# Performance work log

Hardware: AMD Instinct MI355X
Metric: run time of the kernel (lower is better)

Reference implementation:

```python
import jax, jax.numpy as jnp
import numpy as np


def setup_inputs() -> dict:
    ks = iter(jax.random.split(jax.random.key(0), 32))
    B, L, Dm = 16, 256, 512          # batch, seq_len (== len_size), d_model
    N, K, R = 16, 4, 32              # d_state, d_conv, dt_rank = ceil(512/16)
    DI = 2 * Dm                      # d_inner = expand * d_model
    nrm = lambda shape, s=0.02: jax.random.normal(next(ks), shape, jnp.float32) * s
    return {
        "x": jax.random.normal(next(ks), (B, L, Dm), jnp.float32),
        "x_key": jax.random.normal(next(ks), (B, Dm), jnp.float32),
        "in_proj_w": nrm((Dm, 2 * DI)),
        "conv_w": nrm((DI, K), 0.3),                 # depthwise conv kernel
        "conv_b": jnp.zeros((DI,), jnp.float32),
        "x_proj_w": nrm((DI, R + 2 * N)),
        "x_proj_b_w": nrm((DI, R + 2 * N)),
        "x_proj_s_w": nrm((DI, R + 2 * DI)),
        "dt_w": nrm((R, DI)), "dt_bias": jnp.zeros((DI,), jnp.float32),
        "dt_b_w": nrm((R, DI)), "dt_b_bias": jnp.zeros((DI,), jnp.float32),
        "dt_s_w": nrm((R, DI)), "dt_s_bias": jnp.zeros((DI,), jnp.float32),
        "key1_w": nrm((Dm, DI)),
        "key2_w": nrm((N,), 0.1),                    # Linear(1, d_state), no bias
        "keys_w": nrm((Dm, L)),                      # Linear(d_model, len_size)
        "A_log": jnp.log(jnp.arange(1, N + 1, dtype=jnp.float32))[None, :],
        "A_b_log": jnp.log(jnp.arange(1, N + 1, dtype=jnp.float32))[None, :],
        "A_s_log": jnp.log(jnp.arange(1, DI + 1, dtype=jnp.float32))[None, :],
        "D": jnp.ones((DI,), jnp.float32),
        "D_b": jnp.ones((DI,), jnp.float32),
        "D_s": jnp.ones((DI,), jnp.float32),
        "out_proj_w": nrm((DI, Dm)),
    }


def reference(x, x_key, in_proj_w, conv_w, conv_b, x_proj_w, x_proj_b_w, x_proj_s_w,
              dt_w, dt_bias, dt_b_w, dt_b_bias, dt_s_w, dt_s_bias,
              key1_w, key2_w, keys_w, A_log, A_b_log, A_s_log,
              D, D_b, D_s, out_proj_w):
    B, L, _ = x.shape
    R = dt_w.shape[0]
    N = A_log.shape[1]
    DI, K = conv_w.shape

    xz = x @ in_proj_w                                # (B,L,2*DI)
    xc, res = jnp.split(xz, 2, axis=-1)

    # causal depthwise conv (torch pads both sides by K-1 then slices [:L])
    xp = jnp.pad(xc, ((0, 0), (K - 1, 0), (0, 0)))
    u = conv_b + sum(xp[:, k:k + L, :] * conv_w[:, k] for k in range(K))
    u = jax.nn.silu(u)                                # (B,L,DI)

    def proj(W, n):
        p = u @ W
        return jnp.split(p, [R, R + n], axis=-1)

    dr, Bm, Cm = proj(x_proj_w, N)
    drb, Bb, Cb = proj(x_proj_b_w, N)
    drs, Bs, Cs = proj(x_proj_s_w, DI)
    delta = jax.nn.softplus(dr @ dt_w + dt_bias)      # (B,L,DI)
    delta_b = jax.nn.softplus(drb @ dt_b_w + dt_b_bias)
    delta_s = jax.nn.softplus(drs @ dt_s_w + dt_s_bias)

    A = -jnp.exp(A_log[0])                            # (N,)
    Ab = -jnp.exp(A_b_log[0])
    As = -jnp.exp(A_s_log[0])                         # (DI,)

    # initial state: key_proj_2(key_proj_1(x_key)[:, :, None]) -> (B,DI,N)
    s0 = (x_key @ key1_w)[:, :, None] * key2_w

    def temporal(dlt, Aa, Bi, Ci, Dd, reverse):
        dA = jnp.exp(dlt[..., None] * Aa)                           # (B,L,DI,N)
        dBu = dlt[..., None] * Bi[:, :, None, :] * u[..., None]    # (B,L,DI,N)

        def step(s, inp):
            dA_t, dBu_t, C_t = inp
            s = dA_t * s + dBu_t
            return s, jnp.einsum('bdn,bn->bd', s, C_t)

        xs = (jnp.moveaxis(dA, 1, 0), jnp.moveaxis(dBu, 1, 0), jnp.moveaxis(Ci, 1, 0))
        _, ys = jax.lax.scan(step, s0, xs, reverse=reverse)
        return jnp.moveaxis(ys, 0, 1) + u * Dd

    y_f = temporal(delta, A, Bm, Cm, D, False)
    y_b = temporal(delta_b, Ab, Bb, Cb, D_b, True)

    # spatial scan: recurrence over the channel axis, state over sequence positions.
    # torch einsum 'b l d, d n -> b l n' with A_s (1,DI) broadcasts then sums d:
    dA_s = jnp.exp(jnp.sum(delta_s, -1, keepdims=True) * As)        # (B,L,DI)
    dBu_s = jnp.sum(delta_s * u, -1, keepdims=True) * Bs            # (B,L,DI)

    def sstep(s, inp):
        a, bb, c = inp
        s = a * s + bb
        return s, s * c

    _, ys_s = jax.lax.scan(
        sstep, x_key @ keys_w,
        (jnp.moveaxis(dA_s, 2, 0), jnp.moveaxis(dBu_s, 2, 0), jnp.moveaxis(Cs, 2, 0)))
    y_s = jnp.moveaxis(ys_s, 0, 2) + u * D_s                        # (B,L,DI)

    y = y_f + y_b + y_s + res
    return y @ out_proj_w
```

## Files before the change

### kernel.cpp

```cpp
#include <hip/hip_runtime.h>
#include <cstddef>
#include <cstdint>

#define B_   16
#define L_   256
#define DM_  512
#define DI_  1024
#define N_   16
#define R_   32
#define K_   4
#define ROWS (B_ * L_)
#define PP_  256

typedef __attribute__((ext_vector_type(8))) short bf16x8;
typedef __attribute__((ext_vector_type(4))) float f32x4;

__device__ inline unsigned short f2bf(float x) {
    unsigned u = __float_as_uint(x);
    unsigned r = u + 0x7FFFu + ((u >> 16) & 1u);
    return (unsigned short)(r >> 16);
}
__device__ inline float bf2f(unsigned short h) {
    return __uint_as_float(((unsigned)h) << 16);
}

__device__ inline float rowsum16(float x) {
    x += __uint_as_float(__builtin_amdgcn_update_dpp(0, __float_as_uint(x), 0x118, 0xf, 0xf, true));
    x += __uint_as_float(__builtin_amdgcn_update_dpp(0, __float_as_uint(x), 0x114, 0xf, 0xf, true));
    x += __uint_as_float(__builtin_amdgcn_update_dpp(0, __float_as_uint(x), 0x112, 0xf, 0xf, true));
    x += __uint_as_float(__builtin_amdgcn_update_dpp(0, __float_as_uint(x), 0x111, 0xf, 0xf, true));
    return x;
}

#define BM 128
#define BN 128
#define BK 16

__global__ __launch_bounds__(256)
void gemm_f32(const float* __restrict__ A, const float* __restrict__ W,
              float* __restrict__ C, const float* __restrict__ bias,
              int M, int N, int K, int lda, int ldw, int ldc, int mode)
{
    __shared__ float As[BK][BM + 4];
    __shared__ float Ws[BK][BN + 4];
    const int tid = threadIdx.x;
    const int bn = blockIdx.x * BN;
    const int bm = blockIdx.y * BM;

    const int arow = tid >> 2;
    const int ak   = (tid & 3) * 4;
    const int wrow = tid >> 4;
    const int wc   = (tid & 15) * 8;
    const int tx = tid & 15, ty = tid >> 4;

    float acc[8][8];
    #pragma unroll
    for (int i = 0; i < 8; ++i)
        #pragma unroll
        for (int j = 0; j < 8; ++j) acc[i][j] = 0.f;

    for (int kt = 0; kt < K; kt += BK) {
        #pragma unroll
        for (int h = 0; h < 2; ++h) {
            int r = arow + h * 64;
            int grow = bm + r;
            float4 v = make_float4(0.f, 0.f, 0.f, 0.f);
            if (grow < M)
                v = *reinterpret_cast<const float4*>(A + (size_t)grow * lda + kt + ak);
            As[ak + 0][r] = v.x; As[ak + 1][r] = v.y;
            As[ak + 2][r] = v.z; As[ak + 3][r] = v.w;
        }
        #pragma unroll
        for (int h = 0; h < 2; ++h) {
            int col = wc + h * 4;
            int gcol = bn + col;
            float4 v;
            if (gcol + 3 < N) {
                v = *reinterpret_cast<const float4*>(W + (size_t)(kt + wrow) * ldw + gcol);
            } else {
                float t0 = (gcol + 0 < N) ? W[(size_t)(kt + wrow) * ldw + gcol + 0] : 0.f;
                float t1 = (gcol + 1 < N) ? W[(size_t)(kt + wrow) * ldw + gcol + 1] : 0.f;
                float t2 = (gcol + 2 < N) ? W[(size_t)(kt + wrow) * ldw + gcol + 2] : 0.f;
                float t3 = (gcol + 3 < N) ? W[(size_t)(kt + wrow) * ldw + gcol + 3] : 0.f;
                v = make_float4(t0, t1, t2, t3);
            }
            *reinterpret_cast<float4*>(&Ws[wrow][col]) = v;
        }
        __syncthreads();
        #pragma unroll
        for (int k = 0; k < BK; ++k) {
            float av[8], wv[8];
            #pragma unroll
            for (int i = 0; i < 8; ++i) av[i] = As[k][ty * 8 + i];
            #pragma unroll
            for (int j = 0; j < 8; ++j) wv[j] = Ws[k][tx * 8 + j];
            #pragma unroll
            for (int i = 0; i < 8; ++i)
                #pragma unroll
                for (int j = 0; j < 8; ++j)
                    acc[i][j] = fmaf(av[i], wv[j], acc[i][j]);
        }
        __syncthreads();
    }

    #pragma unroll
    for (int i = 0; i < 8; ++i) {
        int r = bm + ty * 8 + i;
        if (r >= M) break;
        #pragma unroll
        for (int j = 0; j < 8; ++j) {
            int cc = bn + tx * 8 + j;
            if (cc < N) {
                float v = acc[i][j];
                if (mode == 1) {
                    v += bias[cc];
                    v = fmaxf(v, 0.f) + log1pf(__expf(-fabsf(v)));
                }
                C[(size_t)r * ldc + cc] = v;
            }
        }
    }
}

#define SBM 128
#define SBN 128
#define SBK 32
#define SLDK 40

__global__ __launch_bounds__(256)
void gemm_split_mfma(const unsigned short* __restrict__ Ahi, const unsigned short* __restrict__ Alo,
                     const unsigned short* __restrict__ Bthi, const unsigned short* __restrict__ Btlo,
                     float* __restrict__ C, int M, int N, int K)
{
    __shared__ unsigned short sAh[SBM][SLDK], sAl[SBM][SLDK];
    __shared__ unsigned short sBh[SBN][SLDK], sBl[SBN][SLDK];
    const int tid = threadIdx.x;
    const int bm = blockIdx.y * SBM;
    const int bn = blockIdx.x * SBN;
    const int w = tid >> 6, lane = tid & 63;
    const int wr = w >> 1, wc = w & 1;
    const int lr = lane & 15, kg = lane >> 4;

    f32x4 acc[4][4];
    #pragma unroll
    for (int i = 0; i < 4; ++i)
        #pragma unroll
        for (int j = 0; j < 4; ++j) acc[i][j] = (f32x4){0.f, 0.f, 0.f, 0.f};

    const int srow0 = tid >> 2;
    const int sks   = (tid & 3) * 8;

    for (int kt = 0; kt < K; kt += SBK) {
        #pragma unroll
        for (int h = 0; h < 2; ++h) {
            int r = srow0 + h * 64;
            size_t ga = (size_t)(bm + r) * K + kt + sks;
            size_t gb = (size_t)(bn + r) * K + kt + sks;
            uint4 vah = *reinterpret_cast<const uint4*>(Ahi + ga);
            uint4 val = *reinterpret_cast<const uint4*>(Alo + ga);
            uint4 vbh = *reinterpret_cast<const uint4*>(Bthi + gb);
            uint4 vbl = *reinterpret_cast<const uint4*>(Btlo + gb);
            *reinterpret_cast<uint4*>(&sAh[r][sks]) = vah;
            *reinterpret_cast<uint4*>(&sAl[r][sks]) = val;
            *reinterpret_cast<uint4*>(&sBh[r][sks]) = vbh;
            *reinterpret_cast<uint4*>(&sBl[r][sks]) = vbl;
        }
        __syncthreads();

        bf16x8 ah[4], al[4], bh[4], bl[4];
        #pragma unroll
        for (int i = 0; i < 4; ++i) {
            ah[i] = *reinterpret_cast<const bf16x8*>(&sAh[wr * 64 + i * 16 + lr][kg * 8]);
            al[i] = *reinterpret_cast<const bf16x8*>(&sAl[wr * 64 + i * 16 + lr][kg * 8]);
            bh[i] = *reinterpret_cast<const bf16x8*>(&sBh[wc * 64 + i * 16 + lr][kg * 8]);
            bl[i] = *reinterpret_cast<const bf16x8*>(&sBl[wc * 64 + i * 16 + lr][kg * 8]);
        }
        #pragma unroll
        for (int i = 0; i < 4; ++i)
            #pragma unroll
            for (int j = 0; j < 4; ++j) {
                acc[i][j] = __builtin_amdgcn_mfma_f32_16x16x32_bf16(ah[i], bh[j], acc[i][j], 0, 0, 0);
                acc[i][j] = __builtin_amdgcn_mfma_f32_16x16x32_bf16(ah[i], bl[j], acc[i][j], 0, 0, 0);
                acc[i][j] = __builtin_amdgcn_mfma_f32_16x16x32_bf16(al[i], bh[j], acc[i][j], 0, 0, 0);
            }
        __syncthreads();
    }

    #pragma unroll
    for (int i = 0; i < 4; ++i)
        #pragma unroll
        for (int j = 0; j < 4; ++j) {
            int col = bn + wc * 64 + j * 16 + lr;
            int rb  = bm + wr * 64 + i * 16 + kg * 4;
            #pragma unroll
            for (int r = 0; r < 4; ++r)
                C[(size_t)(rb + r) * N + col] = acc[i][j][r];
        }
}

__global__ __launch_bounds__(256)
void split_f32(const float* __restrict__ in, unsigned short* __restrict__ hi,
               unsigned short* __restrict__ lo, int n4)
{
    int i = blockIdx.x * 256 + threadIdx.x;
    if (i >= n4) return;
    float4 v = reinterpret_cast<const float4*>(in)[i];
    ushort4 h, l;
    h.x = f2bf(v.x); l.x = f2bf(v.x - bf2f(h.x));
    h.y = f2bf(v.y); l.y = f2bf(v.y - bf2f(h.y));
    h.z = f2bf(v.z); l.z = f2bf(v.z - bf2f(h.z));
    h.w = f2bf(v.w); l.w = f2bf(v.w - bf2f(h.w));
    reinterpret_cast<ushort4*>(hi)[i] = h;
    reinterpret_cast<ushort4*>(lo)[i] = l;
}

__global__ __launch_bounds__(256)
void split_transpose(const float* __restrict__ W, int ldw, int rows, int cols,
                     unsigned short* __restrict__ Thi, unsigned short* __restrict__ Tlo)
{
    __shared__ float t[32][33];
    int k0 = blockIdx.y * 32, n0 = blockIdx.x * 32;
    int tx = threadIdx.x, ty = threadIdx.y;
    #pragma unroll
    for (int i = 0; i < 4; ++i)
        t[ty + i * 8][tx] = W[(size_t)(k0 + ty + i * 8) * ldw + n0 + tx];
    __syncthreads();
    #pragma unroll
    for (int i = 0; i < 4; ++i) {
        int n = ty + i * 8;
        float v = t[tx][n];
        unsigned short h = f2bf(v);
        Thi[(size_t)(n0 + n) * rows + k0 + tx] = h;
        Tlo[(size_t)(n0 + n) * rows + k0 + tx] = f2bf(v - bf2f(h));
    }
}

__global__ __launch_bounds__(256)
void proj_wT(const float* __restrict__ xw, const float* __restrict__ xbw,
             const float* __restrict__ xsw,
             unsigned short* __restrict__ Th, unsigned short* __restrict__ Tl)
{
    int idx = blockIdx.x * 256 + threadIdx.x;
    int k = idx & (DI_ - 1);
    int j = idx >> 10;
    float v = 0.f;
    if (j < 64)       v = xw[(size_t)k * 64 + j];
    else if (j < 128) v = xbw[(size_t)k * 64 + (j - 64)];
    else if (j < 160) v = xsw[(size_t)k * (R_ + 2 * DI_) + (j - 128)];
    unsigned short h = f2bf(v);
    Th[(size_t)j * DI_ + k] = h;
    Tl[(size_t)j * DI_ + k] = f2bf(v - bf2f(h));
}

__global__ __launch_bounds__(256)
void init_state(const float* __restrict__ x_key, const float* __restrict__ key1_w,
                const float* __restrict__ keys_w, float* __restrict__ xk1,
                float* __restrict__ s0sp)
{
    int b = blockIdx.y;
    int col = blockIdx.x * 256 + threadIdx.x;
    __shared__ float xk[DM_];
    for (int i = threadIdx.x; i < DM_; i += 256) xk[i] = x_key[b * DM_ + i];
    __syncthreads();
    float acc = 0.f;
    if (col < DI_) {
        for (int k = 0; k < DM_; ++k)
            acc = fmaf(xk[k], key1_w[(size_t)k * DI_ + col], acc);
        xk1[b * DI_ + col] = acc;
    } else {
        int c = col - DI_;
        for (int k = 0; k < DM_; ++k)
            acc = fmaf(xk[k], keys_w[(size_t)k * L_ + c], acc);
        s0sp[b * L_ + c] = acc;
    }
}

__global__ __launch_bounds__(256)
void conv_silu(const float* __restrict__ xz, const float* __restrict__ conv_w,
               const float* __restrict__ conv_b, float* __restrict__ u)
{
    int idx = blockIdx.x * 256 + threadIdx.x;
    if (idx >= ROWS * DI_) return;
    int d  = idx & (DI_ - 1);
    int rl = idx >> 10;
    int l  = rl & (L_ - 1);
    float acc = conv_b[d];
    #pragma unroll
    for (int k = 0; k < K_; ++k) {
        int ll = l + k - (K_ - 1);
        if (ll >= 0)
            acc = fmaf(xz[(size_t)(rl + k - (K_ - 1)) * (2 * DI_) + d], conv_w[d * K_ + k], acc);
    }
    u[idx] = acc / (1.f + __expf(-acc));
}

__global__ __launch_bounds__(256)
void init_yacc(const float* __restrict__ xz, const float* __restrict__ u,
               const float* __restrict__ D, const float* __restrict__ Db,
               const float* __restrict__ Ds, float* __restrict__ yacc)
{
    int idx = blockIdx.x * 256 + threadIdx.x;
    if (idx >= ROWS * DI_) return;
    int d = idx & (DI_ - 1);
    int row = idx >> 10;
    yacc[idx] = xz[(size_t)row * (2 * DI_) + DI_ + d] + u[idx] * (D[d] + Db[d] + Ds[d]);
}

__global__ __launch_bounds__(256)
void spatial_scalars(const float* __restrict__ pp, const float* __restrict__ Wt,
                     const float* __restrict__ bias, const float* __restrict__ u,
                     float* __restrict__ S1, float* __restrict__ S2)
{
    int r = blockIdx.x;
    int tid = threadIdx.x;
    __shared__ float drsh[R_];
    if (tid < R_) drsh[tid] = pp[(size_t)r * PP_ + 128 + tid];
    __syncthreads();
    float s1 = 0.f, s2 = 0.f;
    #pragma unroll
    for (int j = 0; j < 4; ++j) {
        int d = tid + 256 * j;
        float acc = bias[d];
        #pragma unroll
        for (int k = 0; k < R_; ++k)
            acc = fmaf(drsh[k], Wt[k * DI_ + d], acc);
        float sp = fmaxf(acc, 0.f) + log1pf(__expf(-fabsf(acc)));
        s1 += sp;
        s2 = fmaf(sp, u[(size_t)r * DI_ + d], s2);
    }
    #pragma unroll
    for (int off = 32; off; off >>= 1) {
        s1 += __shfl_down(s1, off, 64);
        s2 += __shfl_down(s2, off, 64);
    }
    __shared__ float red[2][4];
    int wave = tid >> 6, lane = tid & 63;
    if (lane == 0) { red[0][wave] = s1; red[1][wave] = s2; }
    __syncthreads();
    if (tid == 0) {
        S1[r] = red[0][0] + red[0][1] + red[0][2] + red[0][3];
        S2[r] = red[1][0] + red[1][1] + red[1][2] + red[1][3];
    }
}

#define CH 32
#define NCH (L_ / CH)

__global__ __launch_bounds__(256)
void temporal_scan3(const float* __restrict__ delta_f, const float* __restrict__ delta_b,
                    const float* __restrict__ pp,
                    const float* __restrict__ A_log_f, const float* __restrict__ A_log_b,
                    const float* __restrict__ u, const float* __restrict__ xk1,
                    const float* __restrict__ key2, float* __restrict__ yacc)
{
    const int dir = blockIdx.z;
    const float* dlt = dir ? delta_b : delta_f;
    const float* Al  = dir ? A_log_b : A_log_f;
    const int Boff = dir ? 96 : 32;
    const int Coff = dir ? 112 : 48;
    const int b  = blockIdx.y;
    const int d0 = blockIdx.x * 16;
    const int tid = threadIdx.x;
    const int n  = tid & 15, dl = tid >> 4;
    const int lj = tid & 15, lq = tid >> 4;

    __shared__ float4 sDU[2][CH / 2][16];
    __shared__ float4 sBC[2][CH / 2][16];
    __shared__ float2 sY[CH / 2][16];

    float4 rDU, rBC;

    auto gload = [&](int c) {
        int t0 = c * CH + 2 * lq;
        int l0 = dir ? (L_ - 1 - t0) : t0;
        int l1 = dir ? (l0 - 1) : (l0 + 1);
        size_t r0 = (size_t)(b * L_ + l0);
        size_t r1 = (size_t)(b * L_ + l1);
        rDU.x = dlt[r0 * DI_ + d0 + lj];
        rDU.y = u[r0 * DI_ + d0 + lj];
        rDU.z = dlt[r1 * DI_ + d0 + lj];
        rDU.w = u[r1 * DI_ + d0 + lj];
        rBC.x = pp[r0 * PP_ + Boff + lj];
        rBC.y = pp[r0 * PP_ + Coff + lj];
        rBC.z = pp[r1 * PP_ + Boff + lj];
        rBC.w = pp[r1 * PP_ + Coff + lj];
    };
    auto swrite = [&](int bf) {
        sDU[bf][lq][lj] = rDU;
        sBC[bf][lq][lj] = rBC;
    };

    gload(0); swrite(0);
    __syncthreads();

    const float An = -__expf(Al[n]);
    float s = xk1[b * DI_ + d0 + dl] * key2[n];

    for (int c = 0; c < NCH; ++c) {
        int bf = c & 1;
        if (c + 1 < NCH) gload(c + 1);

        #pragma unroll
        for (int q2 = 0; q2 < CH / 2; ++q2) {
            float4 du = sDU[bf][q2][dl];
            float4 bc = sBC[bf][q2][n];
            float dA0 = __expf(An * du.x);
            s = fmaf(dA0, s, du.x * bc.x * du.y);
            float y0 = rowsum16(s * bc.y);
            float dA1 = __expf(An * du.z);
            s = fmaf(dA1, s, du.z * bc.z * du.w);
            float y1 = rowsum16(s * bc.w);
            if (n == 15) sY[q2][dl] = make_float2(y0, y1);
        }
        __syncthreads();
        if (c + 1 < NCH) swrite(bf ^ 1);
        {
            float2 v = sY[lq][lj];
            int t0 = c * CH + 2 * lq;
            int l0 = dir ? (L_ - 1 - t0) : t0;
            int l1 = dir ? (l0 - 1) : (l0 + 1);
            atomicAdd(&yacc[(size_t)(b * L_ + l0) * DI_ + d0 + lj], v.x);
            atomicAdd(&yacc[(size_t)(b * L_ + l1) * DI_ + d0 + lj], v.y);
        }
        __syncthreads();
    }
}

__global__ __launch_bounds__(256)
void spatial_scan(const float* __restrict__ S1b, const float* __restrict__ S2b,
                  const float* __restrict__ Bs, const float* __restrict__ Cs,
                  const float* __restrict__ A_s_log, const float* __restrict__ s0sp,
                  float* __restrict__ yacc)
{
    int wave = threadIdx.x >> 6;
    int lane = threadIdx.x & 63;
    int r = blockIdx.x * 4 + wave;
    float s1 = S1b[r], s2 = S2b[r];
    int dbase = lane * 16;

    float a[16], bb[16];
    float Aloc = 1.f, Bloc = 0.f;
    #pragma unroll
    for (int j = 0; j < 16; ++j) {
        int d = dbase + j;
        float As = -__expf(A_s_log[d]);
        float av = __expf(s1 * As);
        float bv = s2 * Bs[(size_t)r * DI_ + d];
        a[j] = av; bb[j] = bv;
        Bloc = fmaf(av, Bloc, bv);
        Aloc *= av;
    }
    #pragma unroll
    for (int off = 1; off < 64; off <<= 1) {
        float Ap = __shfl_up(Aloc, off, 64);
        float Bp = __shfl_up(Bloc, off, 64);
        if (lane >= off) { Bloc = fmaf(Aloc, Bp, Bloc); Aloc *= Ap; }
    }
    float Aex = __shfl_up(Aloc, 1, 64);
    float Bex = __shfl_up(Bloc, 1, 64);
    if (lane == 0) { Aex = 1.f; Bex = 0.f; }
    float s = fmaf(Aex, s0sp[r], Bex);
    #pragma unroll
    for (int j = 0; j < 16; ++j) {
        int d = dbase + j;
        s = fmaf(a[j], s, bb[j]);
        yacc[(size_t)r * DI_ + d] += s * Cs[(size_t)r * DI_ + d];
    }
}

static inline void launch_gemm(const float* A, const float* W, float* C, const float* bias,
                               int M, int N, int K, int lda, int ldw, int ldc, int mode,
                               hipStream_t stream)
{
    dim3 grid((N + BN - 1) / BN, (M + BM - 1) / BM);
    gemm_f32<<<grid, 256, 0, stream>>>(A, W, C, bias, M, N, K, lda, ldw, ldc, mode);
}

static inline void launch_gemm_mfma(const unsigned short* Ah, const unsigned short* Alo,
                                    const unsigned short* Bh, const unsigned short* Bl,
                                    float* C, int M, int N, int K, hipStream_t stream)
{
    dim3 grid(N / SBN, M / SBM);
    gemm_split_mfma<<<grid, 256, 0, stream>>>(Ah, Alo, Bh, Bl, C, M, N, K);
}

extern "C" void kernel_launch(void* const* d_in, const int* in_sizes, int n_in,
                              void* d_out, int out_size, void* d_ws, size_t ws_size,
                              hipStream_t stream)
{
    const float* x         = (const float*)d_in[0];
    const float* x_key     = (const float*)d_in[1];
    const float* in_proj_w = (const float*)d_in[2];
    const float* conv_w    = (const float*)d_in[3];
    const float* conv_b    = (const float*)d_in[4];
    const float* x_proj_w  = (const float*)d_in[5];
    const float* x_proj_b_w= (const float*)d_in[6];
    const float* x_proj_s_w= (const float*)d_in[7];
    const float* dt_w      = (const float*)d_in[8];
    const float* dt_bias   = (const float*)d_in[9];
    const float* dt_b_w    = (const float*)d_in[10];
    const float* dt_b_bias = (const float*)d_in[11];
    const float* dt_s_w    = (const float*)d_in[12];
    const float* dt_s_bias = (const float*)d_in[13];
    const float* key1_w    = (const float*)d_in[14];
    const float* key2_w    = (const float*)d_in[15];
    const float* keys_w    = (const float*)d_in[16];
    const float* A_log     = (const float*)d_in[17];
    const float* A_b_log   = (const float*)d_in[18];
    const float* A_s_log   = (const float*)d_in[19];
    const float* D         = (const float*)d_in[20];
    const float* D_b       = (const float*)d_in[21];
    const float* D_s       = (const float*)d_in[22];
    const float* out_proj_w= (const float*)d_in[23];

    char* base = (char*)d_ws;
    auto alloc_f = [&](size_t n) { float* p = (float*)base; base += n * 4; return p; };
    auto alloc_h = [&](size_t n) { unsigned short* p = (unsigned short*)base; base += n * 2; return p; };

    float* xz     = alloc_f((size_t)ROWS * 2 * DI_);
    float* u      = alloc_f((size_t)ROWS * DI_);
    float* pp     = alloc_f((size_t)ROWS * PP_);
    float* Bs     = alloc_f((size_t)ROWS * DI_);
    float* Cs     = alloc_f((size_t)ROWS * DI_);
    float* delta  = alloc_f((size_t)ROWS * DI_);
    float* deltab = alloc_f((size_t)ROWS * DI_);
    float* S1     = alloc_f(ROWS);
    float* S2     = alloc_f(ROWS);
    float* xk1    = alloc_f((size_t)B_ * DI_);
    float* s0sp   = alloc_f((size_t)B_ * L_);
    float* yacc   = alloc_f((size_t)ROWS * DI_);
    unsigned short* wscr_h = alloc_h((size_t)2 * DI_ * DM_);
    unsigned short* wscr_l = alloc_h((size_t)2 * DI_ * DM_);

    unsigned short* xhi = (unsigned short*)yacc;
    unsigned short* xlo = xhi + (size_t)ROWS * DM_;
    unsigned short* uhi = (unsigned short*)delta;
    unsigned short* ulo = (unsigned short*)deltab;
    unsigned short* yhi = (unsigned short*)delta;
    unsigned short* ylo = (unsigned short*)deltab;

    float* out = (float*)d_out;
    dim3 tblk(32, 8);

    split_f32<<<(ROWS * DM_ / 4 + 255) / 256, 256, 0, stream>>>(x, xhi, xlo, ROWS * DM_ / 4);
    split_transpose<<<dim3(2 * DI_ / 32, DM_ / 32), tblk, 0, stream>>>(in_proj_w, 2 * DI_, DM_, 2 * DI_, wscr_h, wscr_l);
    launch_gemm_mfma(xhi, xlo, wscr_h, wscr_l, xz, ROWS, 2 * DI_, DM_, stream);
    conv_silu<<<(ROWS * DI_) / 256, 256, 0, stream>>>(xz, conv_w, conv_b, u);
    split_f32<<<(ROWS * DI_ / 4 + 255) / 256, 256, 0, stream>>>(u, uhi, ulo, ROWS * DI_ / 4);
    proj_wT<<<(PP_ * DI_) / 256, 256, 0, stream>>>(x_proj_w, x_proj_b_w, x_proj_s_w, wscr_h, wscr_l);
    launch_gemm_mfma(uhi, ulo, wscr_h, wscr_l, pp, ROWS, PP_, DI_, stream);
    split_transpose<<<dim3(DI_ / 32, DI_ / 32), tblk, 0, stream>>>(x_proj_s_w + 32, R_ + 2 * DI_, DI_, DI_, wscr_h, wscr_l);
    launch_gemm_mfma(uhi, ulo, wscr_h, wscr_l, Bs, ROWS, DI_, DI_, stream);
    split_transpose<<<dim3(DI_ / 32, DI_ / 32), tblk, 0, stream>>>(x_proj_s_w + 32 + DI_, R_ + 2 * DI_, DI_, DI_, wscr_h, wscr_l);
    launch_gemm_mfma(uhi, ulo, wscr_h, wscr_l, Cs, ROWS, DI_, DI_, stream);
    launch_gemm(pp,      dt_w,   delta,  dt_bias,   ROWS, DI_, R_, PP_, DI_, DI_, 1, stream);
    launch_gemm(pp + 64, dt_b_w, deltab, dt_b_bias, ROWS, DI_, R_, PP_, DI_, DI_, 1, stream);
    spatial_scalars<<<ROWS, 256, 0, stream>>>(pp, dt_s_w, dt_s_bias, u, S1, S2);
    {
        dim3 grid((DI_ + L_) / 256, B_);
        init_state<<<grid, 256, 0, stream>>>(x_key, key1_w, keys_w, xk1, s0sp);
    }
    init_yacc<<<(ROWS * DI_) / 256, 256, 0, stream>>>(xz, u, D, D_b, D_s, yacc);
    {
        dim3 grid(DI_ / 16, B_, 2);
        temporal_scan3<<<grid, 256, 0, stream>>>(delta, deltab, pp, A_log, A_b_log,
                                                 u, xk1, key2_w, yacc);
    }
    spatial_scan<<<ROWS / 4, 256, 0, stream>>>(S1, S2, Bs, Cs, A_s_log, s0sp, yacc);
    split_f32<<<(ROWS * DI_ / 4 + 255) / 256, 256, 0, stream>>>(yacc, yhi, ylo, ROWS * DI_ / 4);
    split_transpose<<<dim3(DM_ / 32, DI_ / 32), tblk, 0, stream>>>(out_proj_w, DM_, DI_, DM_, wscr_h, wscr_l);
    launch_gemm_mfma(yhi, ylo, wscr_h, wscr_l, out, ROWS, DM_, DI_, stream);
}
```

Baseline: 580.2 us.

## Fuse conv with bf16 split and yacc init; merge Bs/Cs GEMMs; fuse output split

```diff
diff --git a/kernel.cpp b/kernel.cpp
--- a/kernel.cpp
+++ b/kernel.cpp
@@ -276,8 +276,12 @@
 }
 
 __global__ __launch_bounds__(256)
-void conv_silu(const float* __restrict__ xz, const float* __restrict__ conv_w,
-               const float* __restrict__ conv_b, float* __restrict__ u)
+void conv_silu_pack(const float* __restrict__ xz, const float* __restrict__ conv_w,
+                    const float* __restrict__ conv_b,
+                    const float* __restrict__ D, const float* __restrict__ Db,
+                    const float* __restrict__ Ds,
+                    float* __restrict__ u, unsigned short* __restrict__ uhi,
+                    unsigned short* __restrict__ ulo, float* __restrict__ yacc)
 {
     int idx = blockIdx.x * 256 + threadIdx.x;
     if (idx >= ROWS * DI_) return;
@@ -291,19 +295,12 @@
         if (ll >= 0)
             acc = fmaf(xz[(size_t)(rl + k - (K_ - 1)) * (2 * DI_) + d], conv_w[d * K_ + k], acc);
     }
-    u[idx] = acc / (1.f + __expf(-acc));
-}
-
-__global__ __launch_bounds__(256)
-void init_yacc(const float* __restrict__ xz, const float* __restrict__ u,
-               const float* __restrict__ D, const float* __restrict__ Db,
-               const float* __restrict__ Ds, float* __restrict__ yacc)
-{
-    int idx = blockIdx.x * 256 + threadIdx.x;
-    if (idx >= ROWS * DI_) return;
-    int d = idx & (DI_ - 1);
-    int row = idx >> 10;
-    yacc[idx] = xz[(size_t)row * (2 * DI_) + DI_ + d] + u[idx] * (D[d] + Db[d] + Ds[d]);
+    float uu = acc / (1.f + __expf(-acc));
+    u[idx] = uu;
+    unsigned short h = f2bf(uu);
+    uhi[idx] = h;
+    ulo[idx] = f2bf(uu - bf2f(h));
+    yacc[idx] = xz[(size_t)rl * (2 * DI_) + DI_ + d] + uu * (D[d] + Db[d] + Ds[d]);
 }
 
 __global__ __launch_bounds__(256)
@@ -428,9 +425,10 @@
 
 __global__ __launch_bounds__(256)
 void spatial_scan(const float* __restrict__ S1b, const float* __restrict__ S2b,
-                  const float* __restrict__ Bs, const float* __restrict__ Cs,
+                  const float* __restrict__ bscs,
                   const float* __restrict__ A_s_log, const float* __restrict__ s0sp,
-                  float* __restrict__ yacc)
+                  const float* __restrict__ yacc,
+                  unsigned short* __restrict__ yhi, unsigned short* __restrict__ ylo)
 {
     int wave = threadIdx.x >> 6;
     int lane = threadIdx.x & 63;
@@ -445,7 +443,7 @@
         int d = dbase + j;
         float As = -__expf(A_s_log[d]);
         float av = __expf(s1 * As);
-        float bv = s2 * Bs[(size_t)r * DI_ + d];
+        float bv = s2 * bscs[(size_t)r * 2048 + d];
         a[j] = av; bb[j] = bv;
         Bloc = fmaf(av, Bloc, bv);
         Aloc *= av;
@@ -464,7 +462,10 @@
     for (int j = 0; j < 16; ++j) {
         int d = dbase + j;
         s = fmaf(a[j], s, bb[j]);
-        yacc[(size_t)r * DI_ + d] += s * Cs[(size_t)r * DI_ + d];
+        float v = yacc[(size_t)r * DI_ + d] + s * bscs[(size_t)r * 2048 + 1024 + d];
+        unsigned short h = f2bf(v);
+        yhi[(size_t)r * DI_ + d] = h;
+        ylo[(size_t)r * DI_ + d] = f2bf(v - bf2f(h));
     }
 }
 
@@ -520,8 +521,7 @@
     float* xz     = alloc_f((size_t)ROWS * 2 * DI_);
     float* u      = alloc_f((size_t)ROWS * DI_);
     float* pp     = alloc_f((size_t)ROWS * PP_);
-    float* Bs     = alloc_f((size_t)ROWS * DI_);
-    float* Cs     = alloc_f((size_t)ROWS * DI_);
+    float* bscs   = alloc_f((size_t)ROWS * 2 * DI_);
     float* delta  = alloc_f((size_t)ROWS * DI_);
     float* deltab = alloc_f((size_t)ROWS * DI_);
     float* S1     = alloc_f(ROWS);
@@ -529,8 +529,8 @@
     float* xk1    = alloc_f((size_t)B_ * DI_);
     float* s0sp   = alloc_f((size_t)B_ * L_);
     float* yacc   = alloc_f((size_t)ROWS * DI_);
-    unsigned short* wscr_h = alloc_h((size_t)2 * DI_ * DM_);
-    unsigned short* wscr_l = alloc_h((size_t)2 * DI_ * DM_);
+    unsigned short* wscr_h = alloc_h((size_t)2 * DI_ * DI_ / 1);
+    unsigned short* wscr_l = alloc_h((size_t)2 * DI_ * DI_ / 1);
 
     unsigned short* xhi = (unsigned short*)yacc;
     unsigned short* xlo = xhi + (size_t)ROWS * DM_;
@@ -545,14 +545,12 @@
     split_f32<<<(ROWS * DM_ / 4 + 255) / 256, 256, 0, stream>>>(x, xhi, xlo, ROWS * DM_ / 4);
     split_transpose<<<dim3(2 * DI_ / 32, DM_ / 32), tblk, 0, stream>>>(in_proj_w, 2 * DI_, DM_, 2 * DI_, wscr_h, wscr_l);
     launch_gemm_mfma(xhi, xlo, wscr_h, wscr_l, xz, ROWS, 2 * DI_, DM_, stream);
-    conv_silu<<<(ROWS * DI_) / 256, 256, 0, stream>>>(xz, conv_w, conv_b, u);
-    split_f32<<<(ROWS * DI_ / 4 + 255) / 256, 256, 0, stream>>>(u, uhi, ulo, ROWS * DI_ / 4);
+    conv_silu_pack<<<(ROWS * DI_) / 256, 256, 0, stream>>>(xz, conv_w, conv_b, D, D_b, D_s,
+                                                           u, uhi, ulo, yacc);
     proj_wT<<<(PP_ * DI_) / 256, 256, 0, stream>>>(x_proj_w, x_proj_b_w, x_proj_s_w, wscr_h, wscr_l);
     launch_gemm_mfma(uhi, ulo, wscr_h, wscr_l, pp, ROWS, PP_, DI_, stream);
-    split_transpose<<<dim3(DI_ / 32, DI_ / 32), tblk, 0, stream>>>(x_proj_s_w + 32, R_ + 2 * DI_, DI_, DI_, wscr_h, wscr_l);
-    launch_gemm_mfma(uhi, ulo, wscr_h, wscr_l, Bs, ROWS, DI_, DI_, stream);
-    split_transpose<<<dim3(DI_ / 32, DI_ / 32), tblk, 0, stream>>>(x_proj_s_w + 32 + DI_, R_ + 2 * DI_, DI_, DI_, wscr_h, wscr_l);
-    launch_gemm_mfma(uhi, ulo, wscr_h, wscr_l, Cs, ROWS, DI_, DI_, stream);
+    split_transpose<<<dim3(2 * DI_ / 32, DI_ / 32), tblk, 0, stream>>>(x_proj_s_w + 32, R_ + 2 * DI_, DI_, 2 * DI_, wscr_h, wscr_l);
+    launch_gemm_mfma(uhi, ulo, wscr_h, wscr_l, bscs, ROWS, 2 * DI_, DI_, stream);
     launch_gemm(pp,      dt_w,   delta,  dt_bias,   ROWS, DI_, R_, PP_, DI_, DI_, 1, stream);
     launch_gemm(pp + 64, dt_b_w, deltab, dt_b_bias, ROWS, DI_, R_, PP_, DI_, DI_, 1, stream);
     spatial_scalars<<<ROWS, 256, 0, stream>>>(pp, dt_s_w, dt_s_bias, u, S1, S2);
@@ -560,14 +558,12 @@
         dim3 grid((DI_ + L_) / 256, B_);
         init_state<<<grid, 256, 0, stream>>>(x_key, key1_w, keys_w, xk1, s0sp);
     }
-    init_yacc<<<(ROWS * DI_) / 256, 256, 0, stream>>>(xz, u, D, D_b, D_s, yacc);
     {
         dim3 grid(DI_ / 16, B_, 2);
         temporal_scan3<<<grid, 256, 0, stream>>>(delta, deltab, pp, A_log, A_b_log,
                                                  u, xk1, key2_w, yacc);
     }
-    spatial_scan<<<ROWS / 4, 256, 0, stream>>>(S1, S2, Bs, Cs, A_s_log, s0sp, yacc);
-    split_f32<<<(ROWS * DI_ / 4 + 255) / 256, 256, 0, stream>>>(yacc, yhi, ylo, ROWS * DI_ / 4);
+    spatial_scan<<<ROWS / 4, 256, 0, stream>>>(S1, S2, bscs, A_s_log, s0sp, yacc, yhi, ylo);
     split_transpose<<<dim3(DM_ / 32, DI_ / 32), tblk, 0, stream>>>(out_proj_w, DM_, DI_, DM_, wscr_h, wscr_l);
     launch_gemm_mfma(yhi, ylo, wscr_h, wscr_l, out, ROWS, DM_, DI_, stream);
 }
```

Measured after the change: 628.7 us. +8.3%, slower.
